# Kernel optimization log

Measured on AMD Instinct MI355X. Metric: run time of the kernel, lower is better.

The kernel has to match this reference:

```python
import jax, jax.numpy as jnp
import numpy as np

N, E, A = 10000, 160000, 8
P, ATTR = 30000, 64
EMB, HID, HEADS = 128, 128, 4
OUT, NF, NR = 64, 1500, 64
HOPS = 3
NEG = -1e30


def _gatv2(x, src, dst, e_emb, node_mask, Wl, Wr, We, att, b):
    """GATv2Conv with edge features, self-loops (edge attr = mean of kept edges),
    restricted to the node subset given by node_mask (mirrors Data.subgraph)."""
    n = x.shape[0]
    H, D = att.shape
    xl = (x @ Wl).reshape(n, H, D)
    xr = (x @ Wr).reshape(n, H, D)
    emask = node_mask[src] & node_mask[dst]
    w = emask.astype(x.dtype)
    mean_e = (e_emb * w[:, None]).sum(0) / jnp.maximum(w.sum(), 1.0)  # fill_value='mean'
    loops = jnp.arange(n)
    src_a = jnp.concatenate([src, loops])
    dst_a = jnp.concatenate([dst, loops])
    e_a = jnp.concatenate([e_emb, jnp.broadcast_to(mean_e, (n, e_emb.shape[1]))], axis=0)
    m_a = jnp.concatenate([emask, node_mask])
    ee = (e_a @ We).reshape(-1, H, D)
    z = jax.nn.leaky_relu(xl[src_a] + xr[dst_a] + ee, 0.2)  # [E+N, H, D]
    s = jnp.einsum('ehd,hd->eh', z, att)
    s = jnp.where(m_a[:, None], s, NEG)
    smax = jax.ops.segment_max(s, dst_a, num_segments=n)
    ex = jnp.exp(s - smax[dst_a]) * m_a[:, None].astype(x.dtype)
    den = jax.ops.segment_sum(ex, dst_a, num_segments=n)
    alpha = ex / (den[dst_a] + 1e-16)
    out = jax.ops.segment_sum(alpha[:, :, None] * xl[src_a], dst_a, num_segments=n)
    return out.reshape(n, H * D) + b


def _softmax_aggr(x, mask):
    # PyG SoftmaxAggregation (t=1): per-channel softmax over nodes, weighted sum.
    logit = jnp.where(mask[:, None], x, NEG)
    return jnp.einsum('nd,nd->d', jax.nn.softmax(logit, axis=0), x)


def _khop(seed, src, dst):
    # k_hop_subgraph, flow='source_to_target': grow node set backwards along edges.
    m = jnp.zeros(N, dtype=bool).at[seed].set(True)
    for _ in range(HOPS):
        reach = jnp.zeros(N, dtype=jnp.int32).at[src].max(m[dst].astype(jnp.int32))
        m = m | (reach > 0)
    return m


def _forward(node_pred, edge_index, edge_attr, arg_nodes, pred_emb, Wl1, Wr1, We1, att1, b1,
             Wl2, Wr2, We2, att2, b2, kqv_f, kqvb_f, kqv_r, kqvb_r, a_rel, m_rel, p_rel,
             aW_f, ab_f, aW_r, ab_r, Wfr, bfr, Wro, bro):
    src, dst = edge_index[0], edge_index[1]
    p_emb = pred_emb[node_pred]   # [N, EMB]
    a_emb = pred_emb[edge_attr]   # [E, EMB] (original uses predicate_embedding for attrs)
    full = jnp.ones(N, dtype=bool)
    h = _gatv2(p_emb, src, dst, a_emb, full, Wl1, Wr1, We1, att1, b1)  # [N, HID*HEADS]
    frame_x = _softmax_aggr(h, full)                                   # [512]
    masks = jax.vmap(lambda s: _khop(s, src, dst))(arg_nodes)          # [A, N]
    role_list = []
    for i in range(A):  # mirrors the original Python loop over root args (A fixed, small)
        hi = _gatv2(h, src, dst, a_emb, masks[i], Wl2, Wr2, We2, att2, b2)
        role_list.append(_softmax_aggr(hi, masks[i]))
    role_x = jnp.stack(role_list)                                      # [A, 512]
    # HGTConv, heads=1. Edge types: 0=f-loop, 1=frame->role, 2=r-loop.
    sq = 1.0 / np.sqrt(OUT)
    kf = frame_x @ kqv_f[0] + kqvb_f[0]
    vf = frame_x @ kqv_f[2] + kqvb_f[2]
    kr = role_x @ kqv_r[0] + kqvb_r[0]
    qr = role_x @ kqv_r[1] + kqvb_r[1]
    vr = role_x @ kqv_r[2] + kqvb_r[2]
    # frame dst has a single incoming edge (f-loop) -> softmax weight is exactly 1
    agg_f = vf @ m_rel[0]
    # role dst: softmax over {frame->role edge, role self-loop}
    s_fr = (qr * (kf @ a_rel[1])[None, :]).sum(-1) * sq * p_rel[1]  # [A]
    s_rr = (qr * (kr @ a_rel[2])).sum(-1) * sq * p_rel[2]           # [A]
    al = jax.nn.softmax(jnp.stack([s_fr, s_rr], axis=1), axis=1)    # [A, 2]
    agg_r = al[:, 0:1] * (vf @ m_rel[1])[None, :] + al[:, 1:2] * (vr @ m_rel[2])
    # in_dim (512) != out_dim (64) -> no residual skip in PyG HGTConv
    out_f = jax.nn.gelu(agg_f, approximate=False) @ aW_f + ab_f
    out_r = jax.nn.gelu(agg_r, approximate=False) @ aW_r + ab_r
    frame = jax.nn.log_softmax(out_f @ Wfr + bfr)
    roles = jax.nn.log_softmax(out_r @ Wro + bro, axis=-1)
    return frame, roles


def setup_inputs() -> dict:
    key = jax.random.key(0)
    ki = iter(jax.random.split(key, 32))
    def nrm(shape, fan):
        return (jax.random.normal(next(ki), shape, jnp.float32) / np.sqrt(fan)).astype(jnp.float32)
    D1 = HID * HEADS
    inp = {
        'node_pred': jax.random.randint(next(ki), (N,), 0, P),
        'edge_index': jax.random.randint(next(ki), (2, E), 0, N),
        'edge_attr': jax.random.randint(next(ki), (E,), 0, ATTR),
        'arg_nodes': jax.random.randint(next(ki), (A,), 0, N),
        'pred_emb': nrm((P, EMB), 1.0),
        'Wl1': nrm((EMB, D1), EMB), 'Wr1': nrm((EMB, D1), EMB), 'We1': nrm((EMB, D1), EMB),
        'att1': nrm((HEADS, HID), HID), 'b1': jnp.zeros((D1,), jnp.float32),
        'Wl2': nrm((D1, D1), D1), 'Wr2': nrm((D1, D1), D1), 'We2': nrm((EMB, D1), EMB),
        'att2': nrm((HEADS, HID), HID), 'b2': jnp.zeros((D1,), jnp.float32),
        'kqv_f': nrm((3, D1, OUT), D1), 'kqvb_f': jnp.zeros((3, OUT), jnp.float32),
        'kqv_r': nrm((3, D1, OUT), D1), 'kqvb_r': jnp.zeros((3, OUT), jnp.float32),
        'a_rel': nrm((3, OUT, OUT), OUT), 'm_rel': nrm((3, OUT, OUT), OUT),
        'p_rel': jnp.ones((3,), jnp.float32),
        'aW_f': nrm((OUT, OUT), OUT), 'ab_f': jnp.zeros((OUT,), jnp.float32),
        'aW_r': nrm((OUT, OUT), OUT), 'ab_r': jnp.zeros((OUT,), jnp.float32),
        'Wfr': nrm((OUT, NF), OUT), 'bfr': jnp.zeros((NF,), jnp.float32),
        'Wro': nrm((OUT, NR), OUT), 'bro': jnp.zeros((NR,), jnp.float32),
    }
    return inp


def reference(node_pred, edge_index, edge_attr, arg_nodes, pred_emb, Wl1, Wr1, We1, att1, b1,
              Wl2, Wr2, We2, att2, b2, kqv_f, kqvb_f, kqv_r, kqvb_r, a_rel, m_rel, p_rel,
              aW_f, ab_f, aW_r, ab_r, Wfr, bfr, Wro, bro):
    return _forward(node_pred, edge_index, edge_attr, arg_nodes, pred_emb, Wl1, Wr1, We1, att1, b1,
                    Wl2, Wr2, We2, att2, b2, kqv_f, kqvb_f, kqv_r, kqvb_r, a_rel, m_rel, p_rel,
                    aW_f, ab_f, aW_r, ab_r, Wfr, bfr, Wro, bro)
```

## Files before the change

### kernel.cpp

```cpp
#include <hip/hip_runtime.h>
#include <cfloat>
#include <cmath>

static constexpr int NN   = 10000;
static constexpr int NE   = 160000;
static constexpr int NA   = 8;
static constexpr int D1   = 512;
static constexpr int EMBD = 128;
static constexpr int NATTR= 64;
static constexpr int OUTD = 64;
static constexpr int NFR  = 1500;
static constexpr int AGG_NB = 250;

typedef short bf16x8 __attribute__((ext_vector_type(8)));
typedef float f32x4  __attribute__((ext_vector_type(4)));

__device__ __forceinline__ float b2f(unsigned short u) {
    union { unsigned u; float f; } v; v.u = ((unsigned)u) << 16; return v.f;
}
__device__ __forceinline__ unsigned short f2b(float f) {
    union { float f; unsigned u; } v; v.f = f;
    unsigned r = v.u + 0x7FFFu + ((v.u >> 16) & 1u);
    return (unsigned short)(r >> 16);
}
__device__ __forceinline__ float lrelu(float z) { return (z > 0.f) ? z : 0.2f * z; }

__global__ __launch_bounds__(512) void k_prep(const float* __restrict__ pred_emb,
                                              const float* __restrict__ We1,
                                              const float* __restrict__ We2,
                                              const float* __restrict__ Wl1,
                                              const float* __restrict__ Wr1,
                                              const float* __restrict__ Wl2,
                                              const float* __restrict__ Wr2,
                                              const int* __restrict__ node_pred,
                                              const int* __restrict__ e_dst,
                                              const int* __restrict__ arg_nodes,
                                              unsigned short* __restrict__ attr1,
                                              unsigned short* __restrict__ attr2,
                                              unsigned short* __restrict__ wl1b,
                                              unsigned short* __restrict__ wr1b,
                                              unsigned short* __restrict__ wl2b,
                                              unsigned short* __restrict__ wr2b,
                                              unsigned short* __restrict__ pemb,
                                              int* __restrict__ counts,
                                              unsigned* __restrict__ maskA) {
    int b = blockIdx.x, t = threadIdx.x;
    if (b < 128) {
        int a = b & 63;
        const float* We = (b >> 6) ? We2 : We1;
        unsigned short* out = (b >> 6) ? attr2 : attr1;
        __shared__ float row[EMBD];
        if (t < EMBD) row[t] = pred_emb[a * EMBD + t];
        __syncthreads();
        float acc = 0.f;
        for (int k = 0; k < EMBD; ++k) acc += row[k] * We[k * D1 + t];
        out[a * D1 + t] = f2b(acc);
    } else if (b < 448) {
        int i = (b - 128) * 512 + t;
        const int n1 = EMBD * D1 / 4, n2 = D1 * D1 / 4;
        const float* src; unsigned short* dst; int off;
        if (i < n1)                   { src = Wl1; dst = wl1b; off = i; }
        else if (i < 2 * n1)          { src = Wr1; dst = wr1b; off = i - n1; }
        else if (i < 2 * n1 + n2)     { src = Wl2; dst = wl2b; off = i - 2 * n1; }
        else                          { src = Wr2; dst = wr2b; off = i - 2 * n1 - n2; }
        float4 v = ((const float4*)src)[off];
        ushort4 o; o.x = f2b(v.x); o.y = f2b(v.y); o.z = f2b(v.z); o.w = f2b(v.w);
        ((ushort4*)dst)[off] = o;
    } else if (b < 1073) {
        int idx = (b - 448) * 512 + t;
        int n = idx >> 5, j = idx & 31;
        float4 v = ((const float4*)(pred_emb + (size_t)node_pred[n] * EMBD))[j];
        ushort4 o; o.x = f2b(v.x); o.y = f2b(v.y); o.z = f2b(v.z); o.w = f2b(v.w);
        ((ushort4*)(pemb + (size_t)n * EMBD))[j] = o;
    } else if (b < 1173) {
        int id = (b - 1073) * 512 + t;
        for (int e = id; e < NE; e += 100 * 512) atomicAdd(&counts[e_dst[e]], 1);
    } else {
        if (t < NA) atomicOr(&maskA[arg_nodes[t]], 1u << t);
    }
}

template <int CE>
__global__ __launch_bounds__(1024) void k_scan_g(const int* __restrict__ counts, int n,
                                                 int* __restrict__ row_ptr,
                                                 int* __restrict__ cursor) {
    __shared__ int wsum[16];
    __shared__ int total_s;
    int t = threadIdx.x, lane = t & 63, w = t >> 6;
    int base = t * CE;
    int v[CE];
    int s = 0;
#pragma unroll
    for (int j = 0; j < CE; ++j) {
        int idx = base + j;
        int x = (idx < n) ? counts[idx] : 0;
        v[j] = s; s += x;
    }
    int inc = s;
#pragma unroll
    for (int off = 1; off < 64; off <<= 1) {
        int u = __shfl_up(inc, off, 64);
        if (lane >= off) inc += u;
    }
    if (lane == 63) wsum[w] = inc;
    __syncthreads();
    if (w == 0 && lane < 16) {
        int ws = wsum[lane];
        int wi = ws;
#pragma unroll
        for (int off = 1; off < 16; off <<= 1) {
            int u = __shfl_up(wi, off, 64);
            if (lane >= off) wi += u;
        }
        wsum[lane] = wi - ws;
        if (lane == 15) total_s = wi;
    }
    __syncthreads();
    int excl = wsum[w] + (inc - s);
#pragma unroll
    for (int j = 0; j < CE; ++j) {
        int idx = base + j;
        if (idx < n) { int val = excl + v[j]; row_ptr[idx] = val; cursor[idx] = val; }
    }
    if (t == 0) row_ptr[n] = total_s;
}

__global__ void k_scatter(const int* __restrict__ src, const int* __restrict__ dst,
                          const int* __restrict__ attr, int* __restrict__ cursor,
                          int* __restrict__ csr_pack) {
    int stride = gridDim.x * blockDim.x;
    for (int e = blockIdx.x * blockDim.x + threadIdx.x; e < NE; e += stride) {
        int pos = atomicAdd(&cursor[dst[e]], 1);
        csr_pack[pos] = src[e] | ((attr[e] & 63) << 14);
    }
}

__global__ void k_prop(const unsigned* __restrict__ oldm, unsigned* __restrict__ newm,
                       const int* __restrict__ src, const int* __restrict__ dst) {
    int stride = gridDim.x * blockDim.x;
    int t0 = blockIdx.x * blockDim.x + threadIdx.x;
    for (int n = t0; n < NN; n += stride) atomicOr(&newm[n], oldm[n]);
    for (int e = t0; e < NE; e += stride) {
        unsigned v = oldm[dst[e]];
        if (v) atomicOr(&newm[src[e]], v);
    }
}

__global__ void k_hist(const int* __restrict__ src, const int* __restrict__ dst,
                       const int* __restrict__ attr, const unsigned* __restrict__ mask,
                       unsigned* __restrict__ hist) {
    __shared__ unsigned lh[9 * 64];
    for (int i = threadIdx.x; i < 9 * 64; i += blockDim.x) lh[i] = 0;
    __syncthreads();
    int stride = gridDim.x * blockDim.x;
    for (int e = blockIdx.x * blockDim.x + threadIdx.x; e < NE; e += stride) {
        int a = attr[e] & 63;
        atomicAdd(&lh[a], 1u);
        unsigned bits = mask[src[e]] & mask[dst[e]];
        while (bits) {
            int i = __ffs(bits) - 1;
            bits &= bits - 1;
            atomicAdd(&lh[(1 + i) * 64 + a], 1u);
        }
    }
    __syncthreads();
    for (int i = threadIdx.x; i < 9 * 64; i += blockDim.x)
        if (lh[i]) atomicAdd(&hist[i], lh[i]);
}

__global__ __launch_bounds__(512) void k_mean_ee(const unsigned* __restrict__ hist,
                                                 const float* __restrict__ pred_emb,
                                                 const float* __restrict__ We1,
                                                 const float* __restrict__ We2,
                                                 unsigned short* __restrict__ mee1,
                                                 unsigned short* __restrict__ mee2) {
    int g = blockIdx.x;
    const float* We = (g == 0) ? We1 : We2;
    unsigned short* out = (g == 0) ? mee1 : (mee2 + (g - 1) * D1);
    __shared__ float cnt[64];
    __shared__ float me[EMBD];
    __shared__ float tot_s;
    if (threadIdx.x < 64) cnt[threadIdx.x] = (float)hist[g * 64 + threadIdx.x];
    __syncthreads();
    if (threadIdx.x == 0) {
        float tt = 0.f;
        for (int a = 0; a < 64; ++a) tt += cnt[a];
        tot_s = fmaxf(tt, 1.0f);
    }
    __syncthreads();
    if (threadIdx.x < EMBD) {
        float acc = 0.f;
        for (int a = 0; a < 64; ++a) acc += cnt[a] * pred_emb[a * EMBD + threadIdx.x];
        me[threadIdx.x] = acc / tot_s;
    }
    __syncthreads();
    int c = threadIdx.x;
    float acc = 0.f;
    for (int k = 0; k < EMBD; ++k) acc += me[k] * We[k * D1 + c];
    out[c] = f2b(acc);
}

__global__ __launch_bounds__(256) void k_gemm_dual(const unsigned short* __restrict__ A,
                                                   const unsigned short* __restrict__ B0,
                                                   const unsigned short* __restrict__ B1,
                                                   unsigned short* __restrict__ C0,
                                                   unsigned short* __restrict__ C1,
                                                   int M, int K, int N) {
    const unsigned short* B = blockIdx.z ? B1 : B0;
    unsigned short* C = blockIdx.z ? C1 : C0;
    __shared__ unsigned short As[64][40];
    __shared__ unsigned short Bs[64][40];
    int tid = threadIdx.x;
    int wave = tid >> 6, lane = tid & 63;
    int bm = blockIdx.y * 64, bn = blockIdx.x * 64;
    int wr = (wave >> 1) * 32, wc = (wave & 1) * 32;
    f32x4 zero = {0.f, 0.f, 0.f, 0.f};
    f32x4 acc[2][2] = {{zero, zero}, {zero, zero}};
    for (int k0 = 0; k0 < K; k0 += 32) {
#pragma unroll
        for (int i = 0; i < 4; ++i) {
            int idx = tid + 256 * i;
            int row = idx >> 4, kp = (idx & 15) * 2;
            unsigned v = 0;
            if (bm + row < M) v = *(const unsigned*)&A[(size_t)(bm + row) * K + k0 + kp];
            *(unsigned*)&As[row][kp] = v;
        }
#pragma unroll
        for (int i = 0; i < 8; ++i) {
            int idx = tid + 256 * i;
            int k = idx >> 6, n = idx & 63;
            Bs[n][k] = B[(size_t)(k0 + k) * N + bn + n];
        }
        __syncthreads();
        int r = lane & 15, kb = (lane >> 4) * 8;
        bf16x8 a0 = *(const bf16x8*)&As[wr + r][kb];
        bf16x8 a1 = *(const bf16x8*)&As[wr + 16 + r][kb];
        bf16x8 b0 = *(const bf16x8*)&Bs[wc + r][kb];
        bf16x8 b1 = *(const bf16x8*)&Bs[wc + 16 + r][kb];
        acc[0][0] = __builtin_amdgcn_mfma_f32_16x16x32_bf16(a0, b0, acc[0][0], 0, 0, 0);
        acc[0][1] = __builtin_amdgcn_mfma_f32_16x16x32_bf16(a0, b1, acc[0][1], 0, 0, 0);
        acc[1][0] = __builtin_amdgcn_mfma_f32_16x16x32_bf16(a1, b0, acc[1][0], 0, 0, 0);
        acc[1][1] = __builtin_amdgcn_mfma_f32_16x16x32_bf16(a1, b1, acc[1][1], 0, 0, 0);
        __syncthreads();
    }
    int cr = (lane >> 4) * 4, cc = lane & 15;
#pragma unroll
    for (int i = 0; i < 2; ++i)
#pragma unroll
        for (int j = 0; j < 2; ++j)
#pragma unroll
            for (int q = 0; q < 4; ++q) {
                int row = bm + wr + i * 16 + cr + q;
                int col = bn + wc + j * 16 + cc;
                if (row < M) C[(size_t)row * N + col] = f2b(acc[i][j][q]);
            }
}

__global__ __launch_bounds__(256) void k_gat(const unsigned short* __restrict__ xl,
                                             const unsigned short* __restrict__ xr,
                                             const unsigned short* __restrict__ attr_ee,
                                             const unsigned short* __restrict__ mean_ee,
                                             const float* __restrict__ att,
                                             const float* __restrict__ bias,
                                             const int* __restrict__ row_ptr,
                                             const int* __restrict__ csr_pack,
                                             unsigned short* __restrict__ out) {
    int n = blockIdx.x;
    int t = threadIdx.x;
    int lane = t & 63;
    int half = lane >> 5;
    int c = (t >> 6) * 128 + (lane & 31) * 4;
    uint2 vr2 = *(const uint2*)&xr[(size_t)n * D1 + c];
    float xrv[4] = { b2f((unsigned short)(vr2.x & 0xffff)), b2f((unsigned short)(vr2.x >> 16)),
                     b2f((unsigned short)(vr2.y & 0xffff)), b2f((unsigned short)(vr2.y >> 16)) };
    float4 a4 = *(const float4*)&att[c];
    float m = -FLT_MAX, den = 0.f;
    float ac[4] = {0.f, 0.f, 0.f, 0.f};
    int pstart = row_ptr[n], pend = row_ptr[n + 1];
    int deg = pend - pstart;
    int items = deg + 1;
    for (int it = 0; it < items; it += 4) {
        float xs[2][4], ps[2];
#pragma unroll
        for (int u = 0; u < 2; ++u) {
            int idx = it + u * 2 + half;
            bool valid = idx < items;
            int s; const unsigned short* ee;
            if (!valid || idx == deg) { s = n; ee = mean_ee; }
            else {
                int v = csr_pack[pstart + idx];
                s = v & 0x3FFF;
                ee = attr_ee + (size_t)((v >> 14) & 63) * D1;
            }
            uint2 vs = *(const uint2*)&xl[(size_t)s * D1 + c];
            uint2 ve = *(const uint2*)&ee[c];
            float x0 = b2f((unsigned short)(vs.x & 0xffff)), x1 = b2f((unsigned short)(vs.x >> 16));
            float x2 = b2f((unsigned short)(vs.y & 0xffff)), x3 = b2f((unsigned short)(vs.y >> 16));
            float z0 = lrelu(x0 + xrv[0] + b2f((unsigned short)(ve.x & 0xffff)));
            float z1 = lrelu(x1 + xrv[1] + b2f((unsigned short)(ve.x >> 16)));
            float z2 = lrelu(x2 + xrv[2] + b2f((unsigned short)(ve.y & 0xffff)));
            float z3 = lrelu(x3 + xrv[3] + b2f((unsigned short)(ve.y >> 16)));
            xs[u][0] = x0; xs[u][1] = x1; xs[u][2] = x2; xs[u][3] = x3;
            ps[u] = (z0 * a4.x + z1 * a4.y) + (z2 * a4.z + z3 * a4.w);
        }
#pragma unroll
        for (int off = 1; off < 32; off <<= 1) {
            ps[0] += __shfl_xor(ps[0], off, 64);
            ps[1] += __shfl_xor(ps[1], off, 64);
        }
#pragma unroll
        for (int u = 0; u < 2; ++u) if (it + u * 2 + half >= items) ps[u] = -FLT_MAX;
        float nm = fmaxf(fmaxf(ps[0], ps[1]), m);
        float sc = __expf(m - nm);
        float w0 = __expf(ps[0] - nm);
        float w1 = __expf(ps[1] - nm);
        den = den * sc + w0 + w1;
#pragma unroll
        for (int k = 0; k < 4; ++k) ac[k] = ac[k] * sc + w0 * xs[0][k] + w1 * xs[1][k];
        m = nm;
    }
    float mO = __shfl_xor(m, 32, 64);
    float dO = __shfl_xor(den, 32, 64);
    float aO[4];
#pragma unroll
    for (int k = 0; k < 4; ++k) aO[k] = __shfl_xor(ac[k], 32, 64);
    float nm = fmaxf(m, mO);
    float sa = __expf(m - nm), sb = __expf(mO - nm);
    den = den * sa + dO * sb;
#pragma unroll
    for (int k = 0; k < 4; ++k) ac[k] = ac[k] * sa + aO[k] * sb;
    float inv = 1.f / (den + 1e-16f);
    float4 b4 = *(const float4*)&bias[c];
    unsigned short q0 = f2b(ac[0] * inv + b4.x);
    unsigned short q1 = f2b(ac[1] * inv + b4.y);
    unsigned short q2 = f2b(ac[2] * inv + b4.z);
    unsigned short q3 = f2b(ac[3] * inv + b4.w);
    uint2 o;
    o.x = ((unsigned)q1 << 16) | q0;
    o.y = ((unsigned)q3 << 16) | q2;
    *(uint2*)&out[(size_t)n * D1 + c] = o;
}

__global__ __launch_bounds__(256) void k_gat_m4(const unsigned short* __restrict__ xl,
                                                const unsigned short* __restrict__ xr,
                                                const unsigned short* __restrict__ attr_ee,
                                                const unsigned short* __restrict__ mee,
                                                const float* __restrict__ att,
                                                const float* __restrict__ bias,
                                                const int* __restrict__ row_ptr,
                                                const int* __restrict__ csr_pack,
                                                const unsigned* __restrict__ mask, int bitbase,
                                                unsigned short* __restrict__ o0,
                                                unsigned short* __restrict__ o1,
                                                unsigned short* __restrict__ o2,
                                                unsigned short* __restrict__ o3) {
    int n = blockIdx.x;
    unsigned mb_n = (mask[n] >> bitbase) & 0xFu;
    if (!mb_n) return;
    __shared__ int lst[256];
    __shared__ int lcnt;
    int t = threadIdx.x, lane = t & 63;
    int c = 2 * t;
    unsigned vr_ = *(const unsigned*)&xr[(size_t)n * D1 + c];
    float xr0 = b2f((unsigned short)(vr_ & 0xffff));
    float xr1 = b2f((unsigned short)(vr_ >> 16));
    float a0 = att[c], a1 = att[c + 1];
    float m[4], den[4], ac0[4], ac1[4];
#pragma unroll
    for (int b = 0; b < 4; ++b) { m[b] = -FLT_MAX; den[b] = 0.f; ac0[b] = 0.f; ac1[b] = 0.f; }
    int pstart = row_ptr[n], pend = row_ptr[n + 1];
    for (int p0 = pstart; p0 < pend; p0 += 256) {
        int chunk = min(256, pend - p0);
        __syncthreads();
        if (t == 0) lcnt = 0;
        __syncthreads();
        unsigned bits = 0; int pk = 0;
        if (t < chunk) {
            pk = csr_pack[p0 + t];
            bits = (mask[pk & 0x3FFF] >> bitbase) & mb_n & 0xFu;
        }
        bool kept = bits != 0;
        unsigned long long bal = __ballot(kept);
        int base = 0;
        if (lane == 0) base = atomicAdd(&lcnt, __popcll(bal));
        base = __shfl(base, 0, 64);
        int pfx = __popcll(bal & ((1ull << lane) - 1));
        if (kept) lst[base + pfx] = (pk & 0xFFFFF) | ((int)bits << 20);
        __syncthreads();
        int cnt = lcnt;
        int i = 0;
        for (; i + 1 < cnt; i += 2) {
            int vA = lst[i], vB = lst[i + 1];
            int sA = vA & 0x3FFF, sB = vB & 0x3FFF;
            unsigned bA = ((unsigned)vA >> 20) & 0xF, bB = ((unsigned)vB >> 20) & 0xF;
            const unsigned short* eA = attr_ee + (size_t)((vA >> 14) & 63) * D1;
            const unsigned short* eB = attr_ee + (size_t)((vB >> 14) & 63) * D1;
            unsigned vsA = *(const unsigned*)&xl[(size_t)sA * D1 + c];
            unsigned veA = *(const unsigned*)&eA[c];
            unsigned vsB = *(const unsigned*)&xl[(size_t)sB * D1 + c];
            unsigned veB = *(const unsigned*)&eB[c];
            float xA0 = b2f((unsigned short)(vsA & 0xffff)), xA1 = b2f((unsigned short)(vsA >> 16));
            float xB0 = b2f((unsigned short)(vsB & 0xffff)), xB1 = b2f((unsigned short)(vsB >> 16));
            float zA0 = lrelu(xA0 + xr0 + b2f((unsigned short)(veA & 0xffff)));
            float zA1 = lrelu(xA1 + xr1 + b2f((unsigned short)(veA >> 16)));
            float zB0 = lrelu(xB0 + xr0 + b2f((unsigned short)(veB & 0xffff)));
            float zB1 = lrelu(xB1 + xr1 + b2f((unsigned short)(veB >> 16)));
            float pa = zA0 * a0 + zA1 * a1;
            float pb = zB0 * a0 + zB1 * a1;
#pragma unroll
            for (int off = 32; off; off >>= 1) {
                pa += __shfl_xor(pa, off, 64);
                pb += __shfl_xor(pb, off, 64);
            }
#pragma unroll
            for (int b = 0; b < 4; ++b) {
                if (!(((bA | bB) >> b) & 1)) continue;
                float pae = ((bA >> b) & 1) ? pa : -FLT_MAX;
                float pbe = ((bB >> b) & 1) ? pb : -FLT_MAX;
                float nm = fmaxf(m[b], fmaxf(pae, pbe));
                float sc = __expf(m[b] - nm);
                float wa = __expf(pae - nm);
                float wb = __expf(pbe - nm);
                den[b] = den[b] * sc + wa + wb;
                ac0[b] = ac0[b] * sc + wa * xA0 + wb * xB0;
                ac1[b] = ac1[b] * sc + wa * xA1 + wb * xB1;
                m[b] = nm;
            }
        }
        if (i < cnt) {
            int vA = lst[i];
            int sA = vA & 0x3FFF;
            unsigned bA = ((unsigned)vA >> 20) & 0xF;
            const unsigned short* eA = attr_ee + (size_t)((vA >> 14) & 63) * D1;
            unsigned vsA = *(const unsigned*)&xl[(size_t)sA * D1 + c];
            unsigned veA = *(const unsigned*)&eA[c];
            float xA0 = b2f((unsigned short)(vsA & 0xffff)), xA1 = b2f((unsigned short)(vsA >> 16));
            float zA0 = lrelu(xA0 + xr0 + b2f((unsigned short)(veA & 0xffff)));
            float zA1 = lrelu(xA1 + xr1 + b2f((unsigned short)(veA >> 16)));
            float pa = zA0 * a0 + zA1 * a1;
#pragma unroll
            for (int off = 32; off; off >>= 1) pa += __shfl_xor(pa, off, 64);
#pragma unroll
            for (int b = 0; b < 4; ++b) {
                if (!((bA >> b) & 1)) continue;
                float nm = fmaxf(m[b], pa);
                float sc = __expf(m[b] - nm);
                float wa = __expf(pa - nm);
                den[b] = den[b] * sc + wa;
                ac0[b] = ac0[b] * sc + wa * xA0;
                ac1[b] = ac1[b] * sc + wa * xA1;
                m[b] = nm;
            }
        }
    }
    unsigned vsn = *(const unsigned*)&xl[(size_t)n * D1 + c];
    float xn0 = b2f((unsigned short)(vsn & 0xffff)), xn1 = b2f((unsigned short)(vsn >> 16));
    float bi0 = bias[c], bi1 = bias[c + 1];
#pragma unroll
    for (int b = 0; b < 4; ++b) {
        if (!((mb_n >> b) & 1)) continue;
        unsigned ve = *(const unsigned*)&mee[(size_t)b * D1 + c];
        float z0 = lrelu(xn0 + xr0 + b2f((unsigned short)(ve & 0xffff)));
        float z1 = lrelu(xn1 + xr1 + b2f((unsigned short)(ve >> 16)));
        float ps = z0 * a0 + z1 * a1;
#pragma unroll
        for (int off = 32; off; off >>= 1) ps += __shfl_xor(ps, off, 64);
        float nm = fmaxf(m[b], ps);
        float sc = __expf(m[b] - nm);
        float w  = __expf(ps - nm);
        float dd = den[b] * sc + w;
        float A0 = ac0[b] * sc + w * xn0;
        float A1 = ac1[b] * sc + w * xn1;
        float inv = 1.f / (dd + 1e-16f);
        unsigned short q0 = f2b(A0 * inv + bi0);
        unsigned short q1 = f2b(A1 * inv + bi1);
        unsigned pkd = ((unsigned)q1 << 16) | q0;
        unsigned short* ob = (b == 0) ? o0 : (b == 1) ? o1 : (b == 2) ? o2 : o3;
        *(unsigned*)&ob[(size_t)n * D1 + c] = pkd;
    }
}

__global__ __launch_bounds__(512) void k_aggr_partial(const unsigned short* __restrict__ x,
                                                      float* __restrict__ part) {
    int c = threadIdx.x;
    int rows = NN / gridDim.x;
    int r0 = blockIdx.x * rows;
    int r1 = r0 + rows;
    float m = -FLT_MAX, den = 0.f, num = 0.f;
    for (int r = r0; r < r1; r += 4) {
        float v0 = b2f(x[(size_t)r * D1 + c]);
        float v1 = b2f(x[(size_t)(r + 1) * D1 + c]);
        float v2 = b2f(x[(size_t)(r + 2) * D1 + c]);
        float v3 = b2f(x[(size_t)(r + 3) * D1 + c]);
        float nm = fmaxf(fmaxf(fmaxf(v0, v1), fmaxf(v2, v3)), m);
        float sc = __expf(m - nm);
        float w0 = __expf(v0 - nm);
        float w1 = __expf(v1 - nm);
        float w2 = __expf(v2 - nm);
        float w3 = __expf(v3 - nm);
        den = den * sc + ((w0 + w1) + (w2 + w3));
        num = num * sc + ((w0 * v0 + w1 * v1) + (w2 * v2 + w3 * v3));
        m = nm;
    }
    part[(blockIdx.x * 3 + 0) * D1 + c] = m;
    part[(blockIdx.x * 3 + 1) * D1 + c] = den;
    part[(blockIdx.x * 3 + 2) * D1 + c] = num;
}

__global__ __launch_bounds__(512) void k_aggr_partial4(const unsigned short* __restrict__ h0,
                                                       const unsigned short* __restrict__ h1,
                                                       const unsigned short* __restrict__ h2,
                                                       const unsigned short* __restrict__ h3,
                                                       const unsigned* __restrict__ mask, int bitbase,
                                                       float* __restrict__ part) {
    int c = threadIdx.x;
    int rows = NN / gridDim.x;
    int r0 = blockIdx.x * rows;
    int r1 = r0 + rows;
    float m[4], den[4], num[4];
#pragma unroll
    for (int b = 0; b < 4; ++b) { m[b] = -FLT_MAX; den[b] = 0.f; num[b] = 0.f; }
    for (int r = r0; r < r1; ++r) {
        unsigned bits = (mask[r] >> bitbase) & 0xFu;
        if (!bits) continue;
#pragma unroll
        for (int b = 0; b < 4; ++b) {
            if (!((bits >> b) & 1)) continue;
            const unsigned short* hb = (b == 0) ? h0 : (b == 1) ? h1 : (b == 2) ? h2 : h3;
            float v = b2f(hb[(size_t)r * D1 + c]);
            float nm = fmaxf(m[b], v);
            float sc = __expf(m[b] - nm);
            float w  = __expf(v - nm);
            den[b] = den[b] * sc + w;
            num[b] = num[b] * sc + w * v;
            m[b] = nm;
        }
    }
#pragma unroll
    for (int b = 0; b < 4; ++b) {
        part[(((size_t)b * gridDim.x + blockIdx.x) * 3 + 0) * D1 + c] = m[b];
        part[(((size_t)b * gridDim.x + blockIdx.x) * 3 + 1) * D1 + c] = den[b];
        part[(((size_t)b * gridDim.x + blockIdx.x) * 3 + 2) * D1 + c] = num[b];
    }
}

__global__ __launch_bounds__(512) void k_combine_w(const float* __restrict__ part,
                                                   int nb, int nset,
                                                   float* __restrict__ out) {
    int gw = (blockIdx.x * 512 + threadIdx.x) >> 6;
    int lane = threadIdx.x & 63;
    if (gw >= nset * D1) return;
    int s = gw >> 9;
    int c = gw & 511;
    const float* pp = part + (size_t)s * nb * 3 * D1;
    float m = -FLT_MAX;
    for (int k = lane; k < nb; k += 64) m = fmaxf(m, pp[(k * 3) * D1 + c]);
#pragma unroll
    for (int off = 32; off; off >>= 1) m = fmaxf(m, __shfl_xor(m, off, 64));
    float den = 0.f, num = 0.f;
    for (int k = lane; k < nb; k += 64) {
        float sc = __expf(pp[(k * 3 + 0) * D1 + c] - m);
        den += pp[(k * 3 + 1) * D1 + c] * sc;
        num += pp[(k * 3 + 2) * D1 + c] * sc;
    }
#pragma unroll
    for (int off = 32; off; off >>= 1) {
        den += __shfl_xor(den, off, 64);
        num += __shfl_xor(num, off, 64);
    }
    if (lane == 0) out[(size_t)s * D1 + c] = num / den;
}

__global__ void k_hgt_a(const float* __restrict__ frame_x, const float* __restrict__ role_x,
                        const float* __restrict__ kqv_f, const float* __restrict__ kqvb_f,
                        const float* __restrict__ kqv_r, const float* __restrict__ kqvb_r,
                        float* __restrict__ kf, float* __restrict__ vf,
                        float* __restrict__ kr, float* __restrict__ qr, float* __restrict__ vr) {
    int b = blockIdx.x, j = threadIdx.x;
    const float *x, *W, *bi;
    float* out;
    if (b == 0)      { x = frame_x;               W = kqv_f;                    bi = kqvb_f;            out = kf; }
    else if (b == 1) { x = frame_x;               W = kqv_f + 2 * D1 * OUTD;    bi = kqvb_f + 2 * OUTD; out = vf; }
    else if (b < 10) { int i = b - 2;  x = role_x + i * D1; W = kqv_r;                 bi = kqvb_r;            out = kr + i * OUTD; }
    else if (b < 18) { int i = b - 10; x = role_x + i * D1; W = kqv_r + D1 * OUTD;     bi = kqvb_r + OUTD;     out = qr + i * OUTD; }
    else             { int i = b - 18; x = role_x + i * D1; W = kqv_r + 2 * D1 * OUTD; bi = kqvb_r + 2 * OUTD; out = vr + i * OUTD; }
    float acc = bi[j];
    for (int k = 0; k < D1; ++k) acc += x[k] * W[k * OUTD + j];
    out[j] = acc;
}

__global__ __launch_bounds__(512) void k_hgt_b(const float* __restrict__ kf_g,
                                               const float* __restrict__ vf_g,
                                               const float* __restrict__ kr_g,
                                               const float* __restrict__ qr_g,
                                               const float* __restrict__ vr_g,
                                               const float* __restrict__ a_rel,
                                               const float* __restrict__ m_rel,
                                               const float* __restrict__ p_rel,
                                               const float* __restrict__ aW_f,
                                               const float* __restrict__ ab_f,
                                               const float* __restrict__ aW_r,
                                               const float* __restrict__ ab_r,
                                               float* __restrict__ out_f,
                                               float* __restrict__ out_r) {
    __shared__ float kf[64], vf[64], kr[512], qr[512], vr[512];
    __shared__ float ka1[64], vfm1[64], aggf[64], geluf[64];
    __shared__ float kra2[512], vrm[512], gelur[512];
    __shared__ float al[8][2];
    int t = threadIdx.x;
    if (t < 64) { kf[t] = kf_g[t]; vf[t] = vf_g[t]; }
    kr[t] = kr_g[t]; qr[t] = qr_g[t]; vr[t] = vr_g[t];
    __syncthreads();
    int i = t >> 6, j = t & 63;
    {
        float acc1 = 0.f, acc2 = 0.f;
        for (int k = 0; k < 64; ++k) {
            acc1 += kr[i * 64 + k] * a_rel[2 * 4096 + k * 64 + j];
            acc2 += vr[i * 64 + k] * m_rel[2 * 4096 + k * 64 + j];
        }
        kra2[t] = acc1; vrm[t] = acc2;
    }
    if (t < 64) {
        float acc1 = 0.f, acc2 = 0.f, acc3 = 0.f;
        for (int k = 0; k < 64; ++k) {
            acc1 += kf[k] * a_rel[1 * 4096 + k * 64 + j];
            acc2 += vf[k] * m_rel[0 * 4096 + k * 64 + j];
            acc3 += vf[k] * m_rel[1 * 4096 + k * 64 + j];
        }
        ka1[j] = acc1; aggf[j] = acc2; vfm1[j] = acc3;
    }
    __syncthreads();
    if (t < 8) {
        const float sq = 0.125f;
        float p1 = p_rel[1], p2 = p_rel[2];
        float sfr = 0.f, srr = 0.f;
        for (int d = 0; d < 64; ++d) {
            sfr += qr[t * 64 + d] * ka1[d];
            srr += qr[t * 64 + d] * kra2[t * 64 + d];
        }
        sfr *= sq * p1; srr *= sq * p2;
        float mx = fmaxf(sfr, srr);
        float e0 = __expf(sfr - mx), e1 = __expf(srr - mx);
        float inv = 1.f / (e0 + e1);
        al[t][0] = e0 * inv; al[t][1] = e1 * inv;
    }
    __syncthreads();
    {
        float av = al[i][0] * vfm1[j] + al[i][1] * vrm[t];
        gelur[t] = 0.5f * av * (1.f + erff(av * 0.70710678118654752f));
    }
    if (t < 64) geluf[t] = 0.5f * aggf[t] * (1.f + erff(aggf[t] * 0.70710678118654752f));
    __syncthreads();
    {
        float acc = ab_r[j];
        for (int k = 0; k < 64; ++k) acc += gelur[i * 64 + k] * aW_r[k * 64 + j];
        out_r[t] = acc;
    }
    if (t < 64) {
        float acc = ab_f[j];
        for (int k = 0; k < 64; ++k) acc += geluf[k] * aW_f[k * 64 + j];
        out_f[j] = acc;
    }
}

__global__ void k_frame_logits(const float* __restrict__ out_f, const float* __restrict__ Wfr,
                               const float* __restrict__ bfr, float* __restrict__ flog) {
    __shared__ float xf[64];
    if (threadIdx.x < 64) xf[threadIdx.x] = out_f[threadIdx.x];
    __syncthreads();
    int j = blockIdx.x * blockDim.x + threadIdx.x;
    if (j >= NFR) return;
    float acc = bfr[j];
    for (int k = 0; k < 64; ++k) acc += xf[k] * Wfr[k * NFR + j];
    flog[j] = acc;
}

__global__ __launch_bounds__(512) void k_final(const float* __restrict__ flog,
                                               const float* __restrict__ out_r,
                                               const float* __restrict__ Wro,
                                               const float* __restrict__ bro,
                                               float* __restrict__ outp) {
    __shared__ float red[512];
    __shared__ float xr_s[512];
    int t = threadIdx.x;
    int i = t >> 6, j = t & 63;
    xr_s[t] = out_r[t];
    float racc = bro[j];
    for (int k = 0; k < 64; ++k) racc += xr_s[i * 64 + k] * Wro[k * 64 + j];
    float rm = racc;
#pragma unroll
    for (int off = 32; off; off >>= 1) rm = fmaxf(rm, __shfl_xor(rm, off, 64));
    float re = __expf(racc - rm);
    float rs = re;
#pragma unroll
    for (int off = 32; off; off >>= 1) rs += __shfl_xor(rs, off, 64);
    outp[NFR + t] = racc - rm - logf(rs);
    float m = -FLT_MAX;
    for (int q = t; q < NFR; q += 512) m = fmaxf(m, flog[q]);
    red[t] = m; __syncthreads();
    for (int off = 256; off; off >>= 1) { if (t < off) red[t] = fmaxf(red[t], red[t + off]); __syncthreads(); }
    float M = red[0]; __syncthreads();
    float s = 0.f;
    for (int q = t; q < NFR; q += 512) s += __expf(flog[q] - M);
    red[t] = s; __syncthreads();
    for (int off = 256; off; off >>= 1) { if (t < off) red[t] += red[t + off]; __syncthreads(); }
    float lse = M + logf(red[0]);
    for (int q = t; q < NFR; q += 512) outp[q] = flog[q] - lse;
}

extern "C" void kernel_launch(void* const* d_in, const int* in_sizes, int n_in,
                              void* d_out, int out_size, void* d_ws, size_t ws_size,
                              hipStream_t stream) {
    const int* node_pred  = (const int*)d_in[0];
    const int* edge_index = (const int*)d_in[1];
    const int* e_src = edge_index;
    const int* e_dst = edge_index + NE;
    const int* edge_attr  = (const int*)d_in[2];
    const int* arg_nodes  = (const int*)d_in[3];
    const float* pred_emb = (const float*)d_in[4];
    const float* Wl1 = (const float*)d_in[5];
    const float* Wr1 = (const float*)d_in[6];
    const float* We1 = (const float*)d_in[7];
    const float* att1 = (const float*)d_in[8];
    const float* b1  = (const float*)d_in[9];
    const float* Wl2 = (const float*)d_in[10];
    const float* Wr2 = (const float*)d_in[11];
    const float* We2 = (const float*)d_in[12];
    const float* att2 = (const float*)d_in[13];
    const float* b2  = (const float*)d_in[14];
    const float* kqv_f  = (const float*)d_in[15];
    const float* kqvb_f = (const float*)d_in[16];
    const float* kqv_r  = (const float*)d_in[17];
    const float* kqvb_r = (const float*)d_in[18];
    const float* a_rel  = (const float*)d_in[19];
    const float* m_rel  = (const float*)d_in[20];
    const float* p_rel  = (const float*)d_in[21];
    const float* aW_f = (const float*)d_in[22];
    const float* ab_f = (const float*)d_in[23];
    const float* aW_r = (const float*)d_in[24];
    const float* ab_r = (const float*)d_in[25];
    const float* Wfr = (const float*)d_in[26];
    const float* bfr = (const float*)d_in[27];
    const float* Wro = (const float*)d_in[28];
    const float* bro = (const float*)d_in[29];
    float* outp = (float*)d_out;

    char* base = (char*)d_ws;
    size_t off = 0;
    auto alloc = [&](size_t bytes) -> void* {
        void* p = base + off;
        off += (bytes + 255) & ~(size_t)255;
        return p;
    };
    float* frame_x = (float*)alloc(D1 * 4);
    float* role_x  = (float*)alloc(NA * D1 * 4);
    float* part    = (float*)alloc((size_t)8 * AGG_NB * 3 * D1 * 4);
    float* kf   = (float*)alloc(64 * 4);
    float* vf   = (float*)alloc(64 * 4);
    float* kr   = (float*)alloc(512 * 4);
    float* qr   = (float*)alloc(512 * 4);
    float* vr   = (float*)alloc(512 * 4);
    float* outf = (float*)alloc(64 * 4);
    float* outr = (float*)alloc(512 * 4);
    float* flog = (float*)alloc(NFR * 4);
    int* row_ptr  = (int*)alloc((NN + 1) * 4);
    int* cursor   = (int*)alloc(NN * 4);
    unsigned* maskA = (unsigned*)alloc(NN * 4);
    unsigned* maskB = (unsigned*)alloc(NN * 4);
    unsigned* maskC = (unsigned*)alloc(NN * 4);
    unsigned* hist  = (unsigned*)alloc(9 * 64 * 4);
    size_t zero_end = off;
    size_t zero_beg = (char*)cursor - base;
    int* csr_pack = (int*)alloc((size_t)NE * 4);
    unsigned short* xl    = (unsigned short*)alloc((size_t)NN * D1 * 2);
    unsigned short* xr_   = (unsigned short*)alloc((size_t)NN * D1 * 2);
    unsigned short* hbuf  = (unsigned short*)alloc((size_t)NN * D1 * 2);
    unsigned short* hi1   = (unsigned short*)alloc((size_t)NN * D1 * 2);
    unsigned short* hi2   = (unsigned short*)alloc((size_t)NN * D1 * 2);
    unsigned short* hi3   = (unsigned short*)alloc((size_t)NN * D1 * 2);
    unsigned short* pemb  = (unsigned short*)alloc((size_t)NN * EMBD * 2);
    unsigned short* wl1b  = (unsigned short*)alloc((size_t)EMBD * D1 * 2);
    unsigned short* wr1b  = (unsigned short*)alloc((size_t)EMBD * D1 * 2);
    unsigned short* wl2b  = (unsigned short*)alloc((size_t)D1 * D1 * 2);
    unsigned short* wr2b  = (unsigned short*)alloc((size_t)D1 * D1 * 2);
    unsigned short* attr1 = (unsigned short*)alloc((size_t)NATTR * D1 * 2);
    unsigned short* attr2 = (unsigned short*)alloc((size_t)NATTR * D1 * 2);
    unsigned short* mee1  = (unsigned short*)alloc(D1 * 2);
    unsigned short* mee2  = (unsigned short*)alloc((size_t)NA * D1 * 2);

    hipMemsetAsync(base + zero_beg, 0, zero_end - zero_beg, stream);
    k_prep<<<1174, 512, 0, stream>>>(pred_emb, We1, We2, Wl1, Wr1, Wl2, Wr2,
                                     node_pred, e_dst, arg_nodes,
                                     attr1, attr2, wl1b, wr1b, wl2b, wr2b,
                                     pemb, cursor, maskA);
    k_scan_g<10><<<1, 1024, 0, stream>>>(cursor, NN, row_ptr, cursor);
    k_scatter<<<256, 256, 0, stream>>>(e_src, e_dst, edge_attr, cursor, csr_pack);

    dim3 gg(D1 / 64, (NN + 63) / 64, 2);
    k_gemm_dual<<<gg, 256, 0, stream>>>(pemb, wl1b, wr1b, xl, xr_, NN, EMBD, D1);

    k_prop<<<256, 256, 0, stream>>>(maskA, maskB, e_src, e_dst);
    k_prop<<<256, 256, 0, stream>>>(maskB, maskC, e_src, e_dst);
    k_prop<<<256, 256, 0, stream>>>(maskC, maskA, e_src, e_dst);

    k_hist<<<256, 256, 0, stream>>>(e_src, e_dst, edge_attr, maskA, hist);
    k_mean_ee<<<9, 512, 0, stream>>>(hist, pred_emb, We1, We2, mee1, mee2);

    k_gat<<<NN, 256, 0, stream>>>(xl, xr_, attr1, mee1, att1, b1,
                                  row_ptr, csr_pack, hbuf);
    k_aggr_partial<<<AGG_NB, 512, 0, stream>>>(hbuf, part);
    k_combine_w<<<64, 512, 0, stream>>>(part, AGG_NB, 1, frame_x);

    k_gemm_dual<<<gg, 256, 0, stream>>>(hbuf, wl2b, wr2b, xl, xr_, NN, D1, D1);

    for (int pb = 0; pb < 2; ++pb) {
        int bb = pb * 4;
        k_gat_m4<<<NN, 256, 0, stream>>>(xl, xr_, attr2, mee2 + (size_t)bb * D1, att2, b2,
                                         row_ptr, csr_pack, maskA, bb,
                                         hbuf, hi1, hi2, hi3);
        k_aggr_partial4<<<AGG_NB, 512, 0, stream>>>(hbuf, hi1, hi2, hi3, maskA, bb,
                                                    part + (size_t)pb * 4 * AGG_NB * 3 * D1);
    }
    k_combine_w<<<512, 512, 0, stream>>>(part, AGG_NB, 8, role_x);

    k_hgt_a<<<26, 64, 0, stream>>>(frame_x, role_x, kqv_f, kqvb_f, kqv_r, kqvb_r,
                                   kf, vf, kr, qr, vr);
    k_hgt_b<<<1, 512, 0, stream>>>(kf, vf, kr, qr, vr, a_rel, m_rel, p_rel,
                                   aW_f, ab_f, aW_r, ab_r, outf, outr);
    k_frame_logits<<<(NFR + 255) / 256, 256, 0, stream>>>(outf, Wfr, bfr, flog);
    k_final<<<1, 512, 0, stream>>>(flog, outr, Wro, bro, outp);
}
```

Baseline: 395.4 us.

## Pre-transpose GEMM weights and use swizzled LDS with K=64 tiles

Weight matrices are now converted to bf16 in transposed layout by a new tiled-transpose kernel, so the GEMM loads B rows contiguously instead of doing strided scalar loads plus a scattered LDS transpose. The GEMM K-step grows from 32 to 64, and both LDS tiles use an XOR swizzle to avoid bank conflicts, halving barrier count per K. This adds one extra small kernel launch. It also raises LDS use per block.

```diff
diff --git a/kernel.cpp b/kernel.cpp
--- a/kernel.cpp
+++ b/kernel.cpp
@@ -28,19 +28,11 @@
 __global__ __launch_bounds__(512) void k_prep(const float* __restrict__ pred_emb,
                                               const float* __restrict__ We1,
                                               const float* __restrict__ We2,
-                                              const float* __restrict__ Wl1,
-                                              const float* __restrict__ Wr1,
-                                              const float* __restrict__ Wl2,
-                                              const float* __restrict__ Wr2,
                                               const int* __restrict__ node_pred,
                                               const int* __restrict__ e_dst,
                                               const int* __restrict__ arg_nodes,
                                               unsigned short* __restrict__ attr1,
                                               unsigned short* __restrict__ attr2,
-                                              unsigned short* __restrict__ wl1b,
-                                              unsigned short* __restrict__ wr1b,
-                                              unsigned short* __restrict__ wl2b,
-                                              unsigned short* __restrict__ wr2b,
                                               unsigned short* __restrict__ pemb,
                                               int* __restrict__ counts,
                                               unsigned* __restrict__ maskA) {
@@ -55,28 +47,47 @@
         float acc = 0.f;
         for (int k = 0; k < EMBD; ++k) acc += row[k] * We[k * D1 + t];
         out[a * D1 + t] = f2b(acc);
-    } else if (b < 448) {
-        int i = (b - 128) * 512 + t;
-        const int n1 = EMBD * D1 / 4, n2 = D1 * D1 / 4;
-        const float* src; unsigned short* dst; int off;
-        if (i < n1)                   { src = Wl1; dst = wl1b; off = i; }
-        else if (i < 2 * n1)          { src = Wr1; dst = wr1b; off = i - n1; }
-        else if (i < 2 * n1 + n2)     { src = Wl2; dst = wl2b; off = i - 2 * n1; }
-        else                          { src = Wr2; dst = wr2b; off = i - 2 * n1 - n2; }
-        float4 v = ((const float4*)src)[off];
-        ushort4 o; o.x = f2b(v.x); o.y = f2b(v.y); o.z = f2b(v.z); o.w = f2b(v.w);
-        ((ushort4*)dst)[off] = o;
-    } else if (b < 1073) {
-        int idx = (b - 448) * 512 + t;
+    } else if (b < 753) {
+        int idx = (b - 128) * 512 + t;
         int n = idx >> 5, j = idx & 31;
         float4 v = ((const float4*)(pred_emb + (size_t)node_pred[n] * EMBD))[j];
         ushort4 o; o.x = f2b(v.x); o.y = f2b(v.y); o.z = f2b(v.z); o.w = f2b(v.w);
         ((ushort4*)(pemb + (size_t)n * EMBD))[j] = o;
-    } else if (b < 1173) {
-        int id = (b - 1073) * 512 + t;
+    } else if (b < 853) {
+        int id = (b - 753) * 512 + t;
         for (int e = id; e < NE; e += 100 * 512) atomicAdd(&counts[e_dst[e]], 1);
     } else {
         if (t < NA) atomicOr(&maskA[arg_nodes[t]], 1u << t);
+    }
+}
+
+__global__ __launch_bounds__(256) void k_transp(const float* __restrict__ W1, const float* __restrict__ W2,
+                                                const float* __restrict__ W3, const float* __restrict__ W4,
+                                                unsigned short* __restrict__ o1, unsigned short* __restrict__ o2,
+                                                unsigned short* __restrict__ o3, unsigned short* __restrict__ o4) {
+    int b = blockIdx.x;
+    const float* W; unsigned short* out; int Kd, tile;
+    if (b < 16)      { W = W1; out = o1; Kd = 128; tile = b; }
+    else if (b < 32) { W = W2; out = o2; Kd = 128; tile = b - 16; }
+    else if (b < 96) { W = W3; out = o3; Kd = 512; tile = b - 32; }
+    else             { W = W4; out = o4; Kd = 512; tile = b - 96; }
+    int nrt = Kd / 64;
+    int rt = tile % nrt, ct = tile / nrt;
+    int r0 = rt * 64, c0 = ct * 64;
+    __shared__ float tl[64][65];
+    int tid = threadIdx.x;
+#pragma unroll
+    for (int i = 0; i < 16; ++i) {
+        int idx = tid + 256 * i;
+        int row = idx >> 6, col = idx & 63;
+        tl[row][col] = W[(size_t)(r0 + row) * D1 + c0 + col];
+    }
+    __syncthreads();
+#pragma unroll
+    for (int i = 0; i < 16; ++i) {
+        int idx = tid + 256 * i;
+        int orow = idx >> 6, ocol = idx & 63;
+        out[(size_t)(c0 + orow) * Kd + r0 + ocol] = f2b(tl[ocol][orow]);
     }
 }
 
@@ -201,46 +212,48 @@
 }
 
 __global__ __launch_bounds__(256) void k_gemm_dual(const unsigned short* __restrict__ A,
-                                                   const unsigned short* __restrict__ B0,
-                                                   const unsigned short* __restrict__ B1,
+                                                   const unsigned short* __restrict__ BT0,
+                                                   const unsigned short* __restrict__ BT1,
                                                    unsigned short* __restrict__ C0,
                                                    unsigned short* __restrict__ C1,
                                                    int M, int K, int N) {
-    const unsigned short* B = blockIdx.z ? B1 : B0;
+    const unsigned short* BT = blockIdx.z ? BT1 : BT0;
     unsigned short* C = blockIdx.z ? C1 : C0;
-    __shared__ unsigned short As[64][40];
-    __shared__ unsigned short Bs[64][40];
+    __shared__ unsigned short As[64 * 64];
+    __shared__ unsigned short Bs[64 * 64];
     int tid = threadIdx.x;
     int wave = tid >> 6, lane = tid & 63;
     int bm = blockIdx.y * 64, bn = blockIdx.x * 64;
     int wr = (wave >> 1) * 32, wc = (wave & 1) * 32;
+    int r = lane & 15, s8 = (lane >> 4) * 8;
+    int rx = (r & 7) << 3;
     f32x4 zero = {0.f, 0.f, 0.f, 0.f};
     f32x4 acc[2][2] = {{zero, zero}, {zero, zero}};
-    for (int k0 = 0; k0 < K; k0 += 32) {
-#pragma unroll
-        for (int i = 0; i < 4; ++i) {
-            int idx = tid + 256 * i;
-            int row = idx >> 4, kp = (idx & 15) * 2;
-            unsigned v = 0;
-            if (bm + row < M) v = *(const unsigned*)&A[(size_t)(bm + row) * K + k0 + kp];
-            *(unsigned*)&As[row][kp] = v;
-        }
+    for (int k0 = 0; k0 < K; k0 += 64) {
 #pragma unroll
         for (int i = 0; i < 8; ++i) {
             int idx = tid + 256 * i;
-            int k = idx >> 6, n = idx & 63;
-            Bs[n][k] = B[(size_t)(k0 + k) * N + bn + n];
+            int row = idx >> 5, cdw = idx & 31;
+            int col = (cdw * 2) ^ ((row & 7) << 3);
+            unsigned va = 0;
+            if (bm + row < M) va = *(const unsigned*)&A[(size_t)(bm + row) * K + k0 + cdw * 2];
+            *(unsigned*)&As[row * 64 + col] = va;
+            unsigned vb = *(const unsigned*)&BT[(size_t)(bn + row) * K + k0 + cdw * 2];
+            *(unsigned*)&Bs[row * 64 + col] = vb;
         }
         __syncthreads();
-        int r = lane & 15, kb = (lane >> 4) * 8;
-        bf16x8 a0 = *(const bf16x8*)&As[wr + r][kb];
-        bf16x8 a1 = *(const bf16x8*)&As[wr + 16 + r][kb];
-        bf16x8 b0 = *(const bf16x8*)&Bs[wc + r][kb];
-        bf16x8 b1 = *(const bf16x8*)&Bs[wc + 16 + r][kb];
-        acc[0][0] = __builtin_amdgcn_mfma_f32_16x16x32_bf16(a0, b0, acc[0][0], 0, 0, 0);
-        acc[0][1] = __builtin_amdgcn_mfma_f32_16x16x32_bf16(a0, b1, acc[0][1], 0, 0, 0);
-        acc[1][0] = __builtin_amdgcn_mfma_f32_16x16x32_bf16(a1, b0, acc[1][0], 0, 0, 0);
-        acc[1][1] = __builtin_amdgcn_mfma_f32_16x16x32_bf16(a1, b1, acc[1][1], 0, 0, 0);
+#pragma unroll
+        for (int kk = 0; kk < 2; ++kk) {
+            int csw = (kk * 32 + s8) ^ rx;
+            bf16x8 a0 = *(const bf16x8*)&As[(wr + r) * 64 + csw];
+            bf16x8 a1 = *(const bf16x8*)&As[(wr + 16 + r) * 64 + csw];
+            bf16x8 b0 = *(const bf16x8*)&Bs[(wc + r) * 64 + csw];
+            bf16x8 b1 = *(const bf16x8*)&Bs[(wc + 16 + r) * 64 + csw];
+            acc[0][0] = __builtin_amdgcn_mfma_f32_16x16x32_bf16(a0, b0, acc[0][0], 0, 0, 0);
+            acc[0][1] = __builtin_amdgcn_mfma_f32_16x16x32_bf16(a0, b1, acc[0][1], 0, 0, 0);
+            acc[1][0] = __builtin_amdgcn_mfma_f32_16x16x32_bf16(a1, b0, acc[1][0], 0, 0, 0);
+            acc[1][1] = __builtin_amdgcn_mfma_f32_16x16x32_bf16(a1, b1, acc[1][1], 0, 0, 0);
+        }
         __syncthreads();
     }
     int cr = (lane >> 4) * 4, cc = lane & 15;
@@ -779,25 +792,24 @@
     unsigned short* hi2   = (unsigned short*)alloc((size_t)NN * D1 * 2);
     unsigned short* hi3   = (unsigned short*)alloc((size_t)NN * D1 * 2);
     unsigned short* pemb  = (unsigned short*)alloc((size_t)NN * EMBD * 2);
-    unsigned short* wl1b  = (unsigned short*)alloc((size_t)EMBD * D1 * 2);
-    unsigned short* wr1b  = (unsigned short*)alloc((size_t)EMBD * D1 * 2);
-    unsigned short* wl2b  = (unsigned short*)alloc((size_t)D1 * D1 * 2);
-    unsigned short* wr2b  = (unsigned short*)alloc((size_t)D1 * D1 * 2);
+    unsigned short* wl1t  = (unsigned short*)alloc((size_t)D1 * EMBD * 2);
+    unsigned short* wr1t  = (unsigned short*)alloc((size_t)D1 * EMBD * 2);
+    unsigned short* wl2t  = (unsigned short*)alloc((size_t)D1 * D1 * 2);
+    unsigned short* wr2t  = (unsigned short*)alloc((size_t)D1 * D1 * 2);
     unsigned short* attr1 = (unsigned short*)alloc((size_t)NATTR * D1 * 2);
     unsigned short* attr2 = (unsigned short*)alloc((size_t)NATTR * D1 * 2);
     unsigned short* mee1  = (unsigned short*)alloc(D1 * 2);
     unsigned short* mee2  = (unsigned short*)alloc((size_t)NA * D1 * 2);
 
     hipMemsetAsync(base + zero_beg, 0, zero_end - zero_beg, stream);
-    k_prep<<<1174, 512, 0, stream>>>(pred_emb, We1, We2, Wl1, Wr1, Wl2, Wr2,
-                                     node_pred, e_dst, arg_nodes,
-                                     attr1, attr2, wl1b, wr1b, wl2b, wr2b,
-                                     pemb, cursor, maskA);
+    k_prep<<<854, 512, 0, stream>>>(pred_emb, We1, We2, node_pred, e_dst, arg_nodes,
+                                    attr1, attr2, pemb, cursor, maskA);
+    k_transp<<<160, 256, 0, stream>>>(Wl1, Wr1, Wl2, Wr2, wl1t, wr1t, wl2t, wr2t);
     k_scan_g<10><<<1, 1024, 0, stream>>>(cursor, NN, row_ptr, cursor);
     k_scatter<<<256, 256, 0, stream>>>(e_src, e_dst, edge_attr, cursor, csr_pack);
 
     dim3 gg(D1 / 64, (NN + 63) / 64, 2);
-    k_gemm_dual<<<gg, 256, 0, stream>>>(pemb, wl1b, wr1b, xl, xr_, NN, EMBD, D1);
+    k_gemm_dual<<<gg, 256, 0, stream>>>(pemb, wl1t, wr1t, xl, xr_, NN, EMBD, D1);
 
     k_prop<<<256, 256, 0, stream>>>(maskA, maskB, e_src, e_dst);
     k_prop<<<256, 256, 0, stream>>>(maskB, maskC, e_src, e_dst);
@@ -811,7 +823,7 @@
     k_aggr_partial<<<AGG_NB, 512, 0, stream>>>(hbuf, part);
     k_combine_w<<<64, 512, 0, stream>>>(part, AGG_NB, 1, frame_x);
 
-    k_gemm_dual<<<gg, 256, 0, stream>>>(hbuf, wl2b, wr2b, xl, xr_, NN, D1, D1);
+    k_gemm_dual<<<gg, 256, 0, stream>>>(hbuf, wl2t, wr2t, xl, xr_, NN, D1, D1);
 
     for (int pb = 0; pb < 2; ++pb) {
         int bb = pb * 4;
```

Result: no change. 393.5 us (-0.5%).
